# Kernel optimization log

Measured on AMD Instinct MI355X. Metric: run time of the kernel, lower is better.

The kernel has to match this reference:

```python
import jax, jax.numpy as jnp
import numpy as np

S, B, D, H = 2048, 4, 1024, 16
DK = D // H  # 64


def setup_inputs() -> dict:
    key = jax.random.key(0)
    ks = jax.random.split(key, 11)
    scale = 1.0 / np.sqrt(D)  # xavier-ish init scale
    return {
        "queries": jax.random.normal(ks[0], (S, B, D), jnp.float32),
        "keys": jax.random.normal(ks[1], (S, B, D), jnp.float32),
        "values": jax.random.normal(ks[2], (S, B, D), jnp.float32),
        # torch Linear weights: [out_features, in_features], y = x @ W.T + b
        "Wq": jax.random.normal(ks[3], (D, D), jnp.float32) * scale,
        "bq": jnp.zeros((D,), jnp.float32),
        "Wk": jax.random.normal(ks[4], (D, D), jnp.float32) * scale,
        "bk": jnp.zeros((D,), jnp.float32),
        "Wv": jax.random.normal(ks[5], (D, D), jnp.float32) * scale,
        "bv": jnp.zeros((D,), jnp.float32),
        "Wo": jax.random.normal(ks[6], (D, D), jnp.float32) * scale,
        "bo": jnp.zeros((D,), jnp.float32),
    }


def reference(queries, keys, values, Wq, bq, Wk, bk, Wv, bv, Wo, bo):
    # inputs are seq-first [S, B, D]; module permutes to batch-first
    q_in = jnp.transpose(queries, (1, 0, 2))  # [B, S, D]
    k_in = jnp.transpose(keys, (1, 0, 2))
    v_in = jnp.transpose(values, (1, 0, 2))
    b_s, nq, _ = q_in.shape
    nk = k_in.shape[1]

    # groups=1: grouped view is a no-op -> plain Linear projections
    q = (q_in @ Wq.T + bq).reshape(b_s, nq, H, DK)  # [B, Sq, H, DK]
    k = (k_in @ Wk.T + bk).reshape(b_s, nk, H, DK)
    v = (v_in @ Wv.T + bv).reshape(b_s, nk, H, DK)

    # scores [B, H, Sq, Sk], scaled by 1/sqrt(d_k)
    att = jnp.einsum("bqhd,bkhd->bhqk", q, k) / np.sqrt(DK).astype(np.float32)
    att = jax.nn.softmax(att, axis=-1)
    # dropout p=0.0 (eval semantics): identity

    out = jnp.einsum("bhqk,bkhd->bqhd", att, v).reshape(b_s, nq, H * DK)
    out = out @ Wo.T + bo  # [B, Sq, D]
    return jnp.transpose(out, (1, 0, 2))  # back to [S, B, D]
```

## Files before the change

kernel.cpp:

```cpp
#include <hip/hip_runtime.h>
#include <stdint.h>

#define S_LEN 2048
#define NB    4
#define DMOD  1024
#define NH    16
#define HD    64

typedef float f32x4 __attribute__((ext_vector_type(4)));
typedef float f32x16 __attribute__((ext_vector_type(16)));
typedef short bf16x8 __attribute__((ext_vector_type(8)));
typedef unsigned int u32x4 __attribute__((ext_vector_type(4)));
typedef unsigned short u16;
typedef unsigned int u32;

__device__ __forceinline__ u16 f32_to_bf16(float f) {
  union { float f; unsigned int u; } v; v.f = f;
  unsigned int r = v.u + 0x7fffu + ((v.u >> 16) & 1u);
  return (u16)(r >> 16);
}

__device__ __forceinline__ float fast_exp2(float x) {
#if __has_builtin(__builtin_amdgcn_exp2f)
  return __builtin_amdgcn_exp2f(x);
#else
  return exp2f(x);
#endif
}

typedef __attribute__((address_space(1))) const unsigned int gu32;
typedef __attribute__((address_space(3))) unsigned int lu32;
__device__ __forceinline__ void async_copy16(const void* g, void* l) {
  __builtin_amdgcn_global_load_lds((gu32*)g, (lu32*)l, 16, 0, 0);
}

__global__ __launch_bounds__(256) void convert4_kernel(const float* __restrict__ w0,
                                                       const float* __restrict__ w1,
                                                       const float* __restrict__ w2,
                                                       const float* __restrict__ w3,
                                                       u16* __restrict__ o0, u16* __restrict__ o1,
                                                       u16* __restrict__ o2, u16* __restrict__ o3) {
  const float* in; u16* out;
  switch (blockIdx.y) {
    case 0: in = w0; out = o0; break;
    case 1: in = w1; out = o1; break;
    case 2: in = w2; out = o2; break;
    default: in = w3; out = o3; break;
  }
  int i = (blockIdx.x * 256 + threadIdx.x) * 4;
  float4 v = *(const float4*)(in + i);
  ushort4 o;
  o.x = f32_to_bf16(v.x); o.y = f32_to_bf16(v.y);
  o.z = f32_to_bf16(v.z); o.w = f32_to_bf16(v.w);
  *(ushort4*)(out + i) = o;
}

__global__ __launch_bounds__(256) void gemm_qkv(const float* __restrict__ Xq,
                                                const float* __restrict__ Xk,
                                                const float* __restrict__ Xv,
                                                const u16* __restrict__ Wqb,
                                                const u16* __restrict__ Wkb,
                                                const u16* __restrict__ Wvb,
                                                const float* __restrict__ bq,
                                                const float* __restrict__ bk,
                                                const float* __restrict__ bv,
                                                u16* __restrict__ Qo,
                                                u16* __restrict__ Ko,
                                                u16* __restrict__ Vo,
                                                float qscale) {
  __shared__ u16 a_lds[128 * 32];
  __shared__ u16 b_lds[128 * 32];
  const int tid  = threadIdx.x;
  const int wid  = tid >> 6;
  const int lane = tid & 63;
  const int wm = wid >> 1, wn = wid & 1;
  const int which = blockIdx.z >> 2;
  const int bz = blockIdx.z & 3;
  const int m0 = blockIdx.x * 128;
  const int n0 = blockIdx.y * 128;

  const float* A  = (which == 0) ? Xq : (which == 1) ? Xk : Xv;
  const u16* Bw   = (which == 0) ? Wqb : (which == 1) ? Wkb : Wvb;
  const float* bias = (which == 0) ? bq : (which == 1) ? bk : bv;

  f32x4 acc[4][4] = {};

  for (int kt = 0; kt < 32; ++kt) {
    const int k0 = kt * 32;
    __syncthreads();
    #pragma unroll
    for (int i = 0; i < 2; ++i) {
      int row = wid * 32 + i * 16 + (lane >> 2);
      int sc  = (lane & 3) ^ ((row >> 1) & 3);
      const u16* src = Bw + (size_t)(n0 + row) * 1024 + k0 + sc * 8;
      async_copy16(src, b_lds + wid * 1024 + i * 512);
    }
    {
      int row = tid >> 1, half = tid & 1;
      const float* src = A + ((size_t)(m0 + row) * NB + bz) * 1024 + k0 + half * 16;
      u16 tmp[16];
      #pragma unroll
      for (int i = 0; i < 4; ++i) {
        float4 v = *(const float4*)(src + i * 4);
        tmp[i*4+0] = f32_to_bf16(v.x); tmp[i*4+1] = f32_to_bf16(v.y);
        tmp[i*4+2] = f32_to_bf16(v.z); tmp[i*4+3] = f32_to_bf16(v.w);
      }
      #pragma unroll
      for (int c = 0; c < 2; ++c) {
        int chunk = half * 2 + c;
        int slot  = chunk ^ ((row >> 1) & 3);
        *(int4*)(a_lds + row * 32 + slot * 8) = *(const int4*)(tmp + c * 8);
      }
    }
    asm volatile("s_waitcnt vmcnt(0)" ::: "memory");
    __syncthreads();

    bf16x8 af[4], bfr[4];
    #pragma unroll
    for (int mi = 0; mi < 4; ++mi) {
      int row = wm * 64 + mi * 16 + (lane & 15);
      int ch  = (lane >> 4) ^ ((row >> 1) & 3);
      af[mi] = *(const bf16x8*)(a_lds + row * 32 + ch * 8);
    }
    #pragma unroll
    for (int ni = 0; ni < 4; ++ni) {
      int row = wn * 64 + ni * 16 + (lane & 15);
      int ch  = (lane >> 4) ^ ((row >> 1) & 3);
      bfr[ni] = *(const bf16x8*)(b_lds + row * 32 + ch * 8);
    }
    #pragma unroll
    for (int mi = 0; mi < 4; ++mi)
      #pragma unroll
      for (int ni = 0; ni < 4; ++ni)
        acc[mi][ni] = __builtin_amdgcn_mfma_f32_16x16x32_bf16(af[mi], bfr[ni], acc[mi][ni], 0, 0, 0);
  }

  #pragma unroll
  for (int ni = 0; ni < 4; ++ni) {
    int n = n0 + wn * 64 + ni * 16 + (lane & 15);
    float bv = bias[n];
    int hh = n >> 6, dk = n & 63;
    size_t baseQ = (size_t)(bz * NH + hh) * S_LEN;
    #pragma unroll
    for (int mi = 0; mi < 4; ++mi) {
      int sbase = m0 + wm * 64 + mi * 16 + ((lane >> 4) << 2);
      if (which == 0) {
        #pragma unroll
        for (int r = 0; r < 4; ++r)
          Qo[(baseQ + sbase + r) * HD + dk] = f32_to_bf16((acc[mi][ni][r] + bv) * qscale);
      } else if (which == 1) {
        #pragma unroll
        for (int r = 0; r < 4; ++r) {
          int s = sbase + r;
          int dkp = (((dk >> 2) ^ (s & 15)) << 2) | (dk & 3);
          Ko[(baseQ + s) * HD + dkp] = f32_to_bf16(acc[mi][ni][r] + bv);
        }
      } else {
        int cc = (sbase >> 2) & 15;
        int sp = (sbase & ~63) | (((cc ^ (dk & 15)) << 2));
        size_t idx = ((size_t)(bz * NH + hh) * HD + dk) * S_LEN + sp;
        ushort4 o4;
        o4.x = f32_to_bf16(acc[mi][ni][0] + bv);
        o4.y = f32_to_bf16(acc[mi][ni][1] + bv);
        o4.z = f32_to_bf16(acc[mi][ni][2] + bv);
        o4.w = f32_to_bf16(acc[mi][ni][3] + bv);
        *(ushort4*)(Vo + idx) = o4;
      }
    }
  }
}

__global__ __launch_bounds__(256) void gemm_out(const u16* __restrict__ Ab,
                                                const u16* __restrict__ Bw,
                                                const float* __restrict__ bias,
                                                float* __restrict__ outp) {
  __shared__ u16 a_lds[128 * 32];
  __shared__ u16 b_lds[128 * 32];
  const int tid  = threadIdx.x;
  const int wid  = tid >> 6;
  const int lane = tid & 63;
  const int wm = wid >> 1, wn = wid & 1;
  const int bz = blockIdx.z;
  const int m0 = blockIdx.x * 128;
  const int n0 = blockIdx.y * 128;

  f32x4 acc[4][4] = {};

  for (int kt = 0; kt < 32; ++kt) {
    const int k0 = kt * 32;
    __syncthreads();
    #pragma unroll
    for (int i = 0; i < 2; ++i) {
      int row = wid * 32 + i * 16 + (lane >> 2);
      int sc  = (lane & 3) ^ ((row >> 1) & 3);
      async_copy16(Bw + (size_t)(n0 + row) * 1024 + k0 + sc * 8, b_lds + wid * 1024 + i * 512);
      async_copy16(Ab + ((size_t)bz * S_LEN + m0 + row) * 1024 + k0 + sc * 8, a_lds + wid * 1024 + i * 512);
    }
    asm volatile("s_waitcnt vmcnt(0)" ::: "memory");
    __syncthreads();

    bf16x8 af[4], bfr[4];
    #pragma unroll
    for (int mi = 0; mi < 4; ++mi) {
      int row = wm * 64 + mi * 16 + (lane & 15);
      int ch  = (lane >> 4) ^ ((row >> 1) & 3);
      af[mi] = *(const bf16x8*)(a_lds + row * 32 + ch * 8);
    }
    #pragma unroll
    for (int ni = 0; ni < 4; ++ni) {
      int row = wn * 64 + ni * 16 + (lane & 15);
      int ch  = (lane >> 4) ^ ((row >> 1) & 3);
      bfr[ni] = *(const bf16x8*)(b_lds + row * 32 + ch * 8);
    }
    #pragma unroll
    for (int mi = 0; mi < 4; ++mi)
      #pragma unroll
      for (int ni = 0; ni < 4; ++ni)
        acc[mi][ni] = __builtin_amdgcn_mfma_f32_16x16x32_bf16(af[mi], bfr[ni], acc[mi][ni], 0, 0, 0);
  }

  #pragma unroll
  for (int ni = 0; ni < 4; ++ni) {
    int n = n0 + wn * 64 + ni * 16 + (lane & 15);
    float bv = bias[n];
    #pragma unroll
    for (int mi = 0; mi < 4; ++mi) {
      int sbase = m0 + wm * 64 + mi * 16 + ((lane >> 4) << 2);
      #pragma unroll
      for (int r = 0; r < 4; ++r)
        outp[((size_t)(sbase + r) * NB + bz) * 1024 + n] = acc[mi][ni][r] + bv;
    }
  }
}

__global__ __launch_bounds__(512, 4) void attn_kernel(const u16* __restrict__ Qb,
                                                      const u16* __restrict__ Kb,
                                                      const u16* __restrict__ Vt,
                                                      u16* __restrict__ Oatt) {
  __shared__ u16 kbuf[2][64 * 64];
  __shared__ u16 vbuf[2][64 * 64];
  __shared__ float alds[8][32];
  const int tid = threadIdx.x;
  const int w = tid >> 6, lane = tid & 63;
  const int hi = lane >> 5, l31 = lane & 31;
  const int h = blockIdx.y, b = blockIdx.z;
  const int bh = b * NH + h;
  const int q0 = blockIdx.x * 256 + w * 32;
  const int key = l31 & 15;

  bf16x8 qf[4];
  {
    const u16* qp = Qb + ((size_t)bh * S_LEN + q0 + l31) * HD + hi * 8;
    #pragma unroll
    for (int s = 0; s < 4; ++s) qf[s] = *(const bf16x8*)(qp + s * 16);
  }

  f32x16 acc0 = {}, acc1 = {};
  float m_run = -1e30f, l_run = 0.0f;

  const int rl = w * 8 + (lane >> 3);
  const u16* ksrc = Kb + ((size_t)bh * S_LEN + rl) * HD + (lane & 7) * 8;
  const u16* vsrc = Vt + ((size_t)bh * HD + rl) * S_LEN + (lane & 7) * 8;

  async_copy16(ksrc, &kbuf[0][w * 512]);
  async_copy16(vsrc, &vbuf[0][w * 512]);
  asm volatile("s_waitcnt vmcnt(0)" ::: "memory");
  __syncthreads();

  for (int kb = 0; kb < 32; ++kb) {
    const int cur = kb & 1;
    if (kb + 1 < 32) {
      async_copy16(ksrc + (size_t)(kb + 1) * 64 * HD, &kbuf[cur ^ 1][w * 512]);
      async_copy16(vsrc + (kb + 1) * 64, &vbuf[cur ^ 1][w * 512]);
    }
    const u16* KL = kbuf[cur];
    const u16* VL = vbuf[cur];

    f32x16 pk0 = {}, pk1 = {};
    __builtin_amdgcn_s_setprio(1);
    #pragma unroll
    for (int s = 0; s < 4; ++s) {
      const int c0 = 4 * s + 2 * hi;
      const int p0 = (c0 ^ key) * 4;
      const int p1 = ((c0 + 1) ^ key) * 4;
      uint2 a0 = *(const uint2*)(KL + l31 * 64 + p0);
      uint2 a1 = *(const uint2*)(KL + l31 * 64 + p1);
      uint2 b0 = *(const uint2*)(KL + (32 + l31) * 64 + p0);
      uint2 b1 = *(const uint2*)(KL + (32 + l31) * 64 + p1);
      u32x4 kw0 = {a0.x, a0.y, a1.x, a1.y};
      u32x4 kw1 = {b0.x, b0.y, b1.x, b1.y};
      pk0 = __builtin_amdgcn_mfma_f32_32x32x16_bf16(__builtin_bit_cast(bf16x8, kw0), qf[s], pk0, 0, 0, 0);
      pk1 = __builtin_amdgcn_mfma_f32_32x32x16_bf16(__builtin_bit_cast(bf16x8, kw1), qf[s], pk1, 0, 0, 0);
    }
    __builtin_amdgcn_s_setprio(0);

    float t8[8];
    #pragma unroll
    for (int r = 0; r < 8; ++r)
      t8[r] = fmaxf(fmaxf(pk0[r], pk0[r + 8]), fmaxf(pk1[r], pk1[r + 8]));
    float pm = fmaxf(fmaxf(fmaxf(t8[0], t8[1]), fmaxf(t8[2], t8[3])),
                     fmaxf(fmaxf(t8[4], t8[5]), fmaxf(t8[6], t8[7])));
#if __has_builtin(__builtin_amdgcn_permlane32_swap)
    {
      u32 pmu = __builtin_bit_cast(u32, pm);
      auto sw = __builtin_amdgcn_permlane32_swap(pmu, pmu, false, false);
      float po = __builtin_bit_cast(float, hi ? sw[0] : sw[1]);
      pm = fmaxf(pm, po);
    }
#else
    pm = fmaxf(pm, __shfl_xor(pm, 32));
#endif

    if (!__all(pm <= m_run + 8.0f)) {
      float mn = fmaxf(m_run, pm);
      float al = fast_exp2(m_run - mn);
      m_run = mn;
      l_run *= al;
      if (lane < 32) alds[w][l31] = al;
      #pragma unroll
      for (int r = 0; r < 16; ++r) {
        float av = alds[w][(r & 3) + 8 * (r >> 2) + 4 * hi];
        acc0[r] *= av; acc1[r] *= av;
      }
    }
    #pragma unroll
    for (int r = 0; r < 16; ++r) {
      pk0[r] = fast_exp2(pk0[r] - m_run);
      pk1[r] = fast_exp2(pk1[r] - m_run);
    }

    float rs = 0.0f;
    #pragma unroll
    for (int r = 0; r < 16; ++r) rs += pk0[r] + pk1[r];
#if __has_builtin(__builtin_amdgcn_permlane32_swap)
    {
      u32 ru = __builtin_bit_cast(u32, rs);
      auto sw = __builtin_amdgcn_permlane32_swap(ru, ru, false, false);
      rs += __builtin_bit_cast(float, hi ? sw[0] : sw[1]);
    }
#else
    rs += __shfl_xor(rs, 32);
#endif
    l_run += rs;

    u32 c0v[8], c1v[8];
    #pragma unroll
    for (int i = 0; i < 8; ++i) {
      float a0 = pk0[2 * i], b0 = pk0[2 * i + 1];
      float a1 = pk1[2 * i], b1 = pk1[2 * i + 1];
      asm("v_cvt_pk_bf16_f32 %0, %1, %2" : "=v"(c0v[i]) : "v"(a0), "v"(b0));
      asm("v_cvt_pk_bf16_f32 %0, %1, %2" : "=v"(c1v[i]) : "v"(a1), "v"(b1));
    }

    __builtin_amdgcn_s_setprio(1);
    #pragma unroll
    for (int g = 0; g < 2; ++g) {
      u32 pa0[4], pa1[4];
#if __has_builtin(__builtin_amdgcn_permlane32_swap)
      {
        auto s0 = __builtin_amdgcn_permlane32_swap(c0v[4*g+0], c0v[4*g+2], false, false);
        auto s1 = __builtin_amdgcn_permlane32_swap(c0v[4*g+1], c0v[4*g+3], false, false);
        pa0[0] = s0[0]; pa0[2] = s0[1]; pa0[1] = s1[0]; pa0[3] = s1[1];
        auto t0 = __builtin_amdgcn_permlane32_swap(c1v[4*g+0], c1v[4*g+2], false, false);
        auto t1 = __builtin_amdgcn_permlane32_swap(c1v[4*g+1], c1v[4*g+3], false, false);
        pa1[0] = t0[0]; pa1[2] = t0[1]; pa1[1] = t1[0]; pa1[3] = t1[1];
      }
#else
      {
        u32 x0 = c0v[4*g+0], x1 = c0v[4*g+1], y0 = c0v[4*g+2], y1 = c0v[4*g+3];
        u32 X0 = __shfl_xor((int)x0, 32), X1 = __shfl_xor((int)x1, 32);
        u32 Y0 = __shfl_xor((int)y0, 32), Y1 = __shfl_xor((int)y1, 32);
        pa0[0] = hi ? Y0 : x0; pa0[1] = hi ? Y1 : x1;
        pa0[2] = hi ? y0 : X0; pa0[3] = hi ? y1 : X1;
        x0 = c1v[4*g+0]; x1 = c1v[4*g+1]; y0 = c1v[4*g+2]; y1 = c1v[4*g+3];
        X0 = __shfl_xor((int)x0, 32); X1 = __shfl_xor((int)x1, 32);
        Y0 = __shfl_xor((int)y0, 32); Y1 = __shfl_xor((int)y1, 32);
        pa1[0] = hi ? Y0 : x0; pa1[1] = hi ? Y1 : x1;
        pa1[2] = hi ? y0 : X0; pa1[3] = hi ? y1 : X1;
      }
#endif
      #pragma unroll
      for (int t = 0; t < 2; ++t) {
        const int ks = t == 0 ? g : 2 + g;
        u32x4 pw = t == 0 ? (u32x4){pa0[0], pa0[1], pa0[2], pa0[3]}
                          : (u32x4){pa1[0], pa1[1], pa1[2], pa1[3]};
        bf16x8 paf = __builtin_bit_cast(bf16x8, pw);
        const int c0c = 4 * ks + 2 * hi;
        const int p0 = (c0c ^ key) * 4;
        const int p1 = ((c0c + 1) ^ key) * 4;
        uint2 va0 = *(const uint2*)(VL + l31 * 64 + p0);
        uint2 va1 = *(const uint2*)(VL + l31 * 64 + p1);
        uint2 vb0 = *(const uint2*)(VL + (32 + l31) * 64 + p0);
        uint2 vb1 = *(const uint2*)(VL + (32 + l31) * 64 + p1);
        u32x4 vw0 = {va0.x, va0.y, va1.x, va1.y};
        u32x4 vw1 = {vb0.x, vb0.y, vb1.x, vb1.y};
        acc0 = __builtin_amdgcn_mfma_f32_32x32x16_bf16(paf, __builtin_bit_cast(bf16x8, vw0), acc0, 0, 0, 0);
        acc1 = __builtin_amdgcn_mfma_f32_32x32x16_bf16(paf, __builtin_bit_cast(bf16x8, vw1), acc1, 0, 0, 0);
      }
    }
    __builtin_amdgcn_s_setprio(0);

    asm volatile("s_waitcnt vmcnt(0)" ::: "memory");
    __syncthreads();
  }

  if (lane < 32) alds[w][l31] = l_run;
  #pragma unroll
  for (int r = 0; r < 16; ++r) {
    const int crow = (r & 3) + 8 * (r >> 2) + 4 * hi;
    const int q = q0 + crow;
    u16* op = Oatt + ((size_t)b * S_LEN + q) * DMOD + h * HD;
    const float inv = 1.0f / alds[w][crow];
    op[l31]      = f32_to_bf16(acc0[r] * inv);
    op[32 + l31] = f32_to_bf16(acc1[r] * inv);
  }
}

extern "C" void kernel_launch(void* const* d_in, const int* in_sizes, int n_in,
                              void* d_out, int out_size, void* d_ws, size_t ws_size,
                              hipStream_t stream) {
  const float* Xq = (const float*)d_in[0];
  const float* Xk = (const float*)d_in[1];
  const float* Xv = (const float*)d_in[2];
  const float* Wq = (const float*)d_in[3];
  const float* bq = (const float*)d_in[4];
  const float* Wk = (const float*)d_in[5];
  const float* bk = (const float*)d_in[6];
  const float* Wv = (const float*)d_in[7];
  const float* bv = (const float*)d_in[8];
  const float* Wo = (const float*)d_in[9];
  const float* bo = (const float*)d_in[10];

  u16* Wqb = (u16*)d_ws;
  u16* Wkb = Wqb + (1 << 20);
  u16* Wvb = Wkb + (1 << 20);
  u16* Wob = Wvb + (1 << 20);
  u16* Qb  = Wob + (1 << 20);
  const size_t QKV = (size_t)64 * S_LEN * HD;
  u16* Kb  = Qb + QKV;
  u16* Vt  = Kb + QKV;
  u16* Oat = Vt + QKV;

  convert4_kernel<<<dim3(1024, 4), 256, 0, stream>>>(Wq, Wk, Wv, Wo, Wqb, Wkb, Wvb, Wob);

  gemm_qkv<<<dim3(16, 8, 12), 256, 0, stream>>>(Xq, Xk, Xv, Wqb, Wkb, Wvb,
                                                bq, bk, bv, Qb, Kb, Vt,
                                                0.125f * 1.4426950408889634f);

  attn_kernel<<<dim3(8, 16, 4), 512, 0, stream>>>(Qb, Kb, Vt, Oat);

  gemm_out<<<dim3(16, 8, 4), 256, 0, stream>>>(Oat, Wob, bo, (float*)d_out);
}
```

Baseline: 244.8 us.

## Pre-convert activations to bf16 and flatten projection GEMMs with block swizzle

Adds a pass that converts the fp32 query/key/value inputs to bf16 alongside the weights, so the projection GEMM can load both operands with async global-to-LDS copies instead of converting fp32 inline. The projection and output GEMMs now treat the seq-first input as a flat [S*B, D] matrix, and both use a swizzled block index to group tiles for L2 reuse. The epilogues are rewritten to scatter into per-batch head layouts. This trades an extra full read and write of the activations for a simpler, async-fed main loop.

After: 248.0 us. No clear change (+1.3%).

```diff
diff --git a/kernel.cpp b/kernel.cpp
--- a/kernel.cpp
+++ b/kernel.cpp
@@ -6,6 +6,7 @@
 #define DMOD  1024
 #define NH    16
 #define HD    64
+#define NROWS (S_LEN * NB)
 
 typedef float f32x4 __attribute__((ext_vector_type(4)));
 typedef float f32x16 __attribute__((ext_vector_type(16)));
@@ -34,54 +35,54 @@
   __builtin_amdgcn_global_load_lds((gu32*)g, (lu32*)l, 16, 0, 0);
 }
 
-__global__ __launch_bounds__(256) void convert4_kernel(const float* __restrict__ w0,
-                                                       const float* __restrict__ w1,
-                                                       const float* __restrict__ w2,
-                                                       const float* __restrict__ w3,
-                                                       u16* __restrict__ o0, u16* __restrict__ o1,
-                                                       u16* __restrict__ o2, u16* __restrict__ o3) {
-  const float* in; u16* out;
+__global__ __launch_bounds__(256) void convert_all(
+    const float* __restrict__ w0, const float* __restrict__ w1,
+    const float* __restrict__ w2, const float* __restrict__ w3,
+    const float* __restrict__ x0, const float* __restrict__ x1,
+    const float* __restrict__ x2,
+    u16* __restrict__ o0, u16* __restrict__ o1, u16* __restrict__ o2,
+    u16* __restrict__ o3, u16* __restrict__ o4, u16* __restrict__ o5,
+    u16* __restrict__ o6) {
+  const float* in; u16* out; int n;
   switch (blockIdx.y) {
-    case 0: in = w0; out = o0; break;
-    case 1: in = w1; out = o1; break;
-    case 2: in = w2; out = o2; break;
-    default: in = w3; out = o3; break;
-  }
-  int i = (blockIdx.x * 256 + threadIdx.x) * 4;
-  float4 v = *(const float4*)(in + i);
-  ushort4 o;
-  o.x = f32_to_bf16(v.x); o.y = f32_to_bf16(v.y);
-  o.z = f32_to_bf16(v.z); o.w = f32_to_bf16(v.w);
-  *(ushort4*)(out + i) = o;
-}
-
-__global__ __launch_bounds__(256) void gemm_qkv(const float* __restrict__ Xq,
-                                                const float* __restrict__ Xk,
-                                                const float* __restrict__ Xv,
-                                                const u16* __restrict__ Wqb,
-                                                const u16* __restrict__ Wkb,
-                                                const u16* __restrict__ Wvb,
-                                                const float* __restrict__ bq,
-                                                const float* __restrict__ bk,
-                                                const float* __restrict__ bv,
-                                                u16* __restrict__ Qo,
-                                                u16* __restrict__ Ko,
-                                                u16* __restrict__ Vo,
-                                                float qscale) {
+    case 0: in = w0; out = o0; n = 1 << 20; break;
+    case 1: in = w1; out = o1; n = 1 << 20; break;
+    case 2: in = w2; out = o2; n = 1 << 20; break;
+    case 3: in = w3; out = o3; n = 1 << 20; break;
+    case 4: in = x0; out = o4; n = 1 << 23; break;
+    case 5: in = x1; out = o5; n = 1 << 23; break;
+    default: in = x2; out = o6; n = 1 << 23; break;
+  }
+  for (int i = (blockIdx.x * 256 + threadIdx.x) * 4; i < n; i += gridDim.x * 1024) {
+    float4 v = *(const float4*)(in + i);
+    ushort4 o;
+    o.x = f32_to_bf16(v.x); o.y = f32_to_bf16(v.y);
+    o.z = f32_to_bf16(v.z); o.w = f32_to_bf16(v.w);
+    *(ushort4*)(out + i) = o;
+  }
+}
+
+__global__ __launch_bounds__(256) void gemm_proj(
+    const u16* __restrict__ Xqb, const u16* __restrict__ Xkb, const u16* __restrict__ Xvb,
+    const u16* __restrict__ Wqb, const u16* __restrict__ Wkb, const u16* __restrict__ Wvb,
+    const float* __restrict__ bq, const float* __restrict__ bk, const float* __restrict__ bv,
+    u16* __restrict__ Qo, u16* __restrict__ Ko, u16* __restrict__ Vo, float qscale) {
   __shared__ u16 a_lds[128 * 32];
   __shared__ u16 b_lds[128 * 32];
+  const int lin = blockIdx.x + (blockIdx.y << 6) + (blockIdx.z << 9);
+  const int swz = (lin & 7) * 192 + (lin >> 3);
+  const int m0 = (swz & 63) * 128;
+  const int n0 = ((swz >> 6) & 7) * 128;
+  const int which = swz >> 9;
+
+  const u16* A  = (which == 0) ? Xqb : (which == 1) ? Xkb : Xvb;
+  const u16* Bw = (which == 0) ? Wqb : (which == 1) ? Wkb : Wvb;
+  const float* bias = (which == 0) ? bq : (which == 1) ? bk : bv;
+
   const int tid  = threadIdx.x;
   const int wid  = tid >> 6;
   const int lane = tid & 63;
   const int wm = wid >> 1, wn = wid & 1;
-  const int which = blockIdx.z >> 2;
-  const int bz = blockIdx.z & 3;
-  const int m0 = blockIdx.x * 128;
-  const int n0 = blockIdx.y * 128;
-
-  const float* A  = (which == 0) ? Xq : (which == 1) ? Xk : Xv;
-  const u16* Bw   = (which == 0) ? Wqb : (which == 1) ? Wkb : Wvb;
-  const float* bias = (which == 0) ? bq : (which == 1) ? bk : bv;
 
   f32x4 acc[4][4] = {};
 
@@ -92,25 +93,8 @@
     for (int i = 0; i < 2; ++i) {
       int row = wid * 32 + i * 16 + (lane >> 2);
       int sc  = (lane & 3) ^ ((row >> 1) & 3);
-      const u16* src = Bw + (size_t)(n0 + row) * 1024 + k0 + sc * 8;
-      async_copy16(src, b_lds + wid * 1024 + i * 512);
-    }
-    {
-      int row = tid >> 1, half = tid & 1;
-      const float* src = A + ((size_t)(m0 + row) * NB + bz) * 1024 + k0 + half * 16;
-      u16 tmp[16];
-      #pragma unroll
-      for (int i = 0; i < 4; ++i) {
-        float4 v = *(const float4*)(src + i * 4);
-        tmp[i*4+0] = f32_to_bf16(v.x); tmp[i*4+1] = f32_to_bf16(v.y);
-        tmp[i*4+2] = f32_to_bf16(v.z); tmp[i*4+3] = f32_to_bf16(v.w);
-      }
-      #pragma unroll
-      for (int c = 0; c < 2; ++c) {
-        int chunk = half * 2 + c;
-        int slot  = chunk ^ ((row >> 1) & 3);
-        *(int4*)(a_lds + row * 32 + slot * 8) = *(const int4*)(tmp + c * 8);
-      }
+      async_copy16(Bw + (size_t)(n0 + row) * 1024 + k0 + sc * 8, b_lds + wid * 1024 + i * 512);
+      async_copy16(A + (size_t)(m0 + row) * 1024 + k0 + sc * 8, a_lds + wid * 1024 + i * 512);
     }
     asm volatile("s_waitcnt vmcnt(0)" ::: "memory");
     __syncthreads();
@@ -140,31 +124,27 @@
     int n = n0 + wn * 64 + ni * 16 + (lane & 15);
     float bv = bias[n];
     int hh = n >> 6, dk = n & 63;
-    size_t baseQ = (size_t)(bz * NH + hh) * S_LEN;
     #pragma unroll
     for (int mi = 0; mi < 4; ++mi) {
       int sbase = m0 + wm * 64 + mi * 16 + ((lane >> 4) << 2);
+      int s = sbase >> 2;
       if (which == 0) {
         #pragma unroll
         for (int r = 0; r < 4; ++r)
-          Qo[(baseQ + sbase + r) * HD + dk] = f32_to_bf16((acc[mi][ni][r] + bv) * qscale);
+          Qo[((size_t)(r * NH + hh) * S_LEN + s) * HD + dk] =
+              f32_to_bf16((acc[mi][ni][r] + bv) * qscale);
       } else if (which == 1) {
+        int dkp = (((dk >> 2) ^ (s & 15)) << 2) | (dk & 3);
         #pragma unroll
-        for (int r = 0; r < 4; ++r) {
-          int s = sbase + r;
-          int dkp = (((dk >> 2) ^ (s & 15)) << 2) | (dk & 3);
-          Ko[(baseQ + s) * HD + dkp] = f32_to_bf16(acc[mi][ni][r] + bv);
-        }
+        for (int r = 0; r < 4; ++r)
+          Ko[((size_t)(r * NH + hh) * S_LEN + s) * HD + dkp] =
+              f32_to_bf16(acc[mi][ni][r] + bv);
       } else {
-        int cc = (sbase >> 2) & 15;
-        int sp = (sbase & ~63) | (((cc ^ (dk & 15)) << 2));
-        size_t idx = ((size_t)(bz * NH + hh) * HD + dk) * S_LEN + sp;
-        ushort4 o4;
-        o4.x = f32_to_bf16(acc[mi][ni][0] + bv);
-        o4.y = f32_to_bf16(acc[mi][ni][1] + bv);
-        o4.z = f32_to_bf16(acc[mi][ni][2] + bv);
-        o4.w = f32_to_bf16(acc[mi][ni][3] + bv);
-        *(ushort4*)(Vo + idx) = o4;
+        int sp = (s & ~63) | ((((s >> 2) & 15) ^ (dk & 15)) << 2) | (s & 3);
+        #pragma unroll
+        for (int r = 0; r < 4; ++r)
+          Vo[((size_t)(r * NH + hh) * HD + dk) * S_LEN + sp] =
+              f32_to_bf16(acc[mi][ni][r] + bv);
       }
     }
   }
@@ -176,13 +156,14 @@
                                                 float* __restrict__ outp) {
   __shared__ u16 a_lds[128 * 32];
   __shared__ u16 b_lds[128 * 32];
+  const int lin = blockIdx.x + (blockIdx.y << 6);
+  const int swz = (lin & 7) * 64 + (lin >> 3);
+  const int m0 = (swz & 63) * 128;
+  const int n0 = (swz >> 6) * 128;
   const int tid  = threadIdx.x;
   const int wid  = tid >> 6;
   const int lane = tid & 63;
   const int wm = wid >> 1, wn = wid & 1;
-  const int bz = blockIdx.z;
-  const int m0 = blockIdx.x * 128;
-  const int n0 = blockIdx.y * 128;
 
   f32x4 acc[4][4] = {};
 
@@ -194,7 +175,7 @@
       int row = wid * 32 + i * 16 + (lane >> 2);
       int sc  = (lane & 3) ^ ((row >> 1) & 3);
       async_copy16(Bw + (size_t)(n0 + row) * 1024 + k0 + sc * 8, b_lds + wid * 1024 + i * 512);
-      async_copy16(Ab + ((size_t)bz * S_LEN + m0 + row) * 1024 + k0 + sc * 8, a_lds + wid * 1024 + i * 512);
+      async_copy16(Ab + (size_t)(m0 + row) * 1024 + k0 + sc * 8, a_lds + wid * 1024 + i * 512);
     }
     asm volatile("s_waitcnt vmcnt(0)" ::: "memory");
     __syncthreads();
@@ -227,8 +208,11 @@
     for (int mi = 0; mi < 4; ++mi) {
       int sbase = m0 + wm * 64 + mi * 16 + ((lane >> 4) << 2);
       #pragma unroll
-      for (int r = 0; r < 4; ++r)
-        outp[((size_t)(sbase + r) * NB + bz) * 1024 + n] = acc[mi][ni][r] + bv;
+      for (int r = 0; r < 4; ++r) {
+        int m = sbase + r;
+        int bb = m >> 11, s = m & 2047;
+        outp[((size_t)(s * NB + bb)) * 1024 + n] = acc[mi][ni][r] + bv;
+      }
     }
   }
 }
@@ -440,14 +424,18 @@
   u16* Kb  = Qb + QKV;
   u16* Vt  = Kb + QKV;
   u16* Oat = Vt + QKV;
-
-  convert4_kernel<<<dim3(1024, 4), 256, 0, stream>>>(Wq, Wk, Wv, Wo, Wqb, Wkb, Wvb, Wob);
-
-  gemm_qkv<<<dim3(16, 8, 12), 256, 0, stream>>>(Xq, Xk, Xv, Wqb, Wkb, Wvb,
+  u16* Xqb = Oat + QKV;
+  u16* Xkb = Xqb + QKV;
+  u16* Xvb = Xkb + QKV;
+
+  convert_all<<<dim3(2048, 7), 256, 0, stream>>>(Wq, Wk, Wv, Wo, Xq, Xk, Xv,
+                                                 Wqb, Wkb, Wvb, Wob, Xqb, Xkb, Xvb);
+
+  gemm_proj<<<dim3(64, 8, 3), 256, 0, stream>>>(Xqb, Xkb, Xvb, Wqb, Wkb, Wvb,
                                                 bq, bk, bv, Qb, Kb, Vt,
                                                 0.125f * 1.4426950408889634f);
 
   attn_kernel<<<dim3(8, 16, 4), 512, 0, stream>>>(Qb, Kb, Vt, Oat);
 
-  gemm_out<<<dim3(16, 8, 4), 256, 0, stream>>>(Oat, Wob, bo, (float*)d_out);
-}
+  gemm_out<<<dim3(64, 8), 256, 0, stream>>>(Oat, Wob, bo, (float*)d_out);
+}
```
